# Kernel tuning notes

Hardware: AMD Instinct MI355X
Metric: run time of the kernel (lower is better)

## Reference

```python
import jax, jax.numpy as jnp
import numpy as np

FIRST_BIN = 0.0
LAST_BIN = 1.0
NBINS = 32
ER = 1.0
RATIO = 2.5066  # ~sqrt(2*pi), constant from the original module
SIGMA = (LAST_BIN - FIRST_BIN) / NBINS


def setup_inputs() -> dict:
    key = jax.random.key(0)
    x = jax.random.uniform(key, (8, 8, 256, 256), dtype=jnp.float32)
    bin_centers = jnp.linspace(FIRST_BIN, LAST_BIN, NBINS, dtype=jnp.float32)
    return {"x": x, "bin_centers": bin_centers}


def reference(x, bin_centers):
    # x: [B, C, H, W]; bin_centers: [nbins]
    B, C, H, W = x.shape
    nbins = bin_centers.shape[0]
    xc = jnp.clip(x, bin_centers[0], bin_centers[-1])
    # Gaussian soft binning: [B, C, H, W, nbins]
    diff = xc[..., None] - bin_centers
    w = (ER / RATIO) * jnp.exp(-(diff * diff) / (2.0 * SIGMA * SIGMA))
    # per-channel permute + concat == transpose then merge (C, nbins) -> C*nbins
    w = jnp.transpose(w, (0, 1, 4, 2, 3)).reshape(B, C * nbins, H, W)
    # pooling='sum' over dims [2,3] with keepdims
    return jnp.sum(w, axis=(2, 3), keepdims=True)
```

## Files before the change

### kernel.cpp

```cpp
#include <hip/hip_runtime.h>


#define NBINS        32
#define CHUNKS_PER_IMG 32
#define PX           2048

__device__ __forceinline__ float fast_exp2(float x) { return __builtin_amdgcn_exp2f(x); }

__global__ __launch_bounds__(256) void hist_partial(const float* __restrict__ x,
                                                    float* __restrict__ partial)
{
    __shared__ float2 sta[PX];
    __shared__ float  red[NBINS * 8];

    const int tid = threadIdx.x;
    const int bid = blockIdx.x;
    const int img   = bid >> 5;
    const int chunk = bid & (CHUNKS_PER_IMG - 1);
    const float* __restrict__ xp = x + (size_t)img * 65536 + (size_t)chunk * PX;

    const float C2L = -0.76863882f;

    #pragma unroll
    for (int k = 0; k < PX / 256; ++k) {
        int p = tid + 256 * k;
        float xv = xp[p];
        float xc = fminf(fmaxf(xv, 0.0f), 1.0f);
        float t  = xc * 31.0f;
        sta[p] = make_float2(t, C2L * t * t);
    }
    __syncthreads();

    const int j = tid & 31;
    const int g = tid >> 5;
    const float jf = (float)j;
    const float bj = 1.53727764f * jf;
    const float cj = C2L * jf * jf;

    const float4* __restrict__ sp = (const float4*)&sta[g * (PX >> 3)];
    float acc0 = 0.0f, acc1 = 0.0f;
    #pragma unroll 4
    for (int m = 0; m < (PX >> 4); ++m) {
        float4 v = sp[m];
        float a0 = fmaf(bj, v.x, v.y) + cj;
        float a1 = fmaf(bj, v.z, v.w) + cj;
        acc0 += fast_exp2(a0);
        acc1 += fast_exp2(a1);
    }

    red[j * 8 + g] = acc0 + acc1;
    __syncthreads();
    if (tid < NBINS) {
        float s = 0.0f;
        #pragma unroll
        for (int r = 0; r < 8; ++r) s += red[tid * 8 + r];
        partial[bid * NBINS + tid] = 0.39894678f * s;
    }
}

__global__ __launch_bounds__(256) void hist_reduce(const float* __restrict__ partial,
                                                   float* __restrict__ out)
{
    int o = blockIdx.x * 256 + threadIdx.x;
    int img = o >> 5;
    int bin = o & 31;
    float s = 0.0f;
    #pragma unroll
    for (int k = 0; k < CHUNKS_PER_IMG; ++k)
        s += partial[(img * CHUNKS_PER_IMG + k) * NBINS + bin];
    out[o] = s;
}

extern "C" void kernel_launch(void* const* d_in, const int* in_sizes, int n_in,
                              void* d_out, int out_size, void* d_ws, size_t ws_size,
                              hipStream_t stream)
{
    (void)in_sizes; (void)n_in; (void)out_size; (void)ws_size;
    const float* x = (const float*)d_in[0];
    float* out     = (float*)d_out;
    float* partial = (float*)d_ws;

    hist_partial<<<64 * CHUNKS_PER_IMG, 256, 0, stream>>>(x, partial);
    hist_reduce<<<8, 256, 0, stream>>>(partial, out);
}
```

Before: 79.19 us.

## Replace per-pixel Gaussian evaluation with fine sub-bin histogram and Taylor-corrected convolution

New measurement: 71.31 us. -10.0%, faster.

```diff
diff --git a/kernel.cpp b/kernel.cpp
--- a/kernel.cpp
+++ b/kernel.cpp
@@ -1,60 +1,75 @@
 #include <hip/hip_runtime.h>
 
 
-#define NBINS        32
-#define CHUNKS_PER_IMG 32
-#define PX           2048
+#define NBINS 32
+#define NBLK  512
+#define PXB   8192
+#define NSUB  2049
 
 __device__ __forceinline__ float fast_exp2(float x) { return __builtin_amdgcn_exp2f(x); }
 
 __global__ __launch_bounds__(256) void hist_partial(const float* __restrict__ x,
                                                     float* __restrict__ partial)
 {
-    __shared__ float2 sta[PX];
-    __shared__ float  red[NBINS * 8];
+    __shared__ unsigned long long hist[NSUB];
+    __shared__ float red[NBINS * 8];
 
     const int tid = threadIdx.x;
     const int bid = blockIdx.x;
-    const int img   = bid >> 5;
-    const int chunk = bid & (CHUNKS_PER_IMG - 1);
-    const float* __restrict__ xp = x + (size_t)img * 65536 + (size_t)chunk * PX;
 
-    const float C2L = -0.76863882f;
+    for (int i = tid; i < NSUB; i += 256) hist[i] = 0ull;
+    __syncthreads();
 
+    const float4* __restrict__ xv = (const float4*)(x + (size_t)bid * PXB);
     #pragma unroll
-    for (int k = 0; k < PX / 256; ++k) {
-        int p = tid + 256 * k;
-        float xv = xp[p];
-        float xc = fminf(fmaxf(xv, 0.0f), 1.0f);
-        float t  = xc * 31.0f;
-        sta[p] = make_float2(t, C2L * t * t);
+    for (int k = 0; k < PXB / 1024; ++k) {
+        float4 v = xv[tid + 256 * k];
+        #pragma unroll
+        for (int e = 0; e < 4; ++e) {
+            float xr = (e == 0) ? v.x : (e == 1) ? v.y : (e == 2) ? v.z : v.w;
+            float xc = fminf(fmaxf(xr, 0.0f), 1.0f);
+            float gf = xc * 2048.0f;
+            float sf = rintf(gf);
+            int   s  = (int)sf;
+            int   qi = (int)rintf((gf - sf) * 65536.0f) + 32768;
+            atomicAdd(&hist[s], ((unsigned long long)1 << 32) | (unsigned)qi);
+        }
     }
     __syncthreads();
 
     const int j = tid & 31;
     const int g = tid >> 5;
     const float jf = (float)j;
-    const float bj = 1.53727764f * jf;
-    const float cj = C2L * jf * jf;
 
-    const float4* __restrict__ sp = (const float4*)&sta[g * (PX >> 3)];
-    float acc0 = 0.0f, acc1 = 0.0f;
-    #pragma unroll 4
-    for (int m = 0; m < (PX >> 4); ++m) {
-        float4 v = sp[m];
-        float a0 = fmaf(bj, v.x, v.y) + cj;
-        float a1 = fmaf(bj, v.z, v.w) + cj;
-        acc0 += fast_exp2(a0);
-        acc1 += fast_exp2(a1);
+    const float DT  = 0.015136719f;
+    const float C2L = -0.7686388f;
+    const float M2C = -1.0655567f;
+    const float QS  = 2.3096800e-7f;
+    const float R0  = 0.39894678f;
+
+    int s_lo = (int)ceilf((jf - 4.5f) * 66.064516f);
+    int s_hi = (int)floorf((jf + 4.5f) * 66.064516f);
+    if (s_lo < 0) s_lo = 0;
+    if (s_hi > NSUB - 1) s_hi = NSUB - 1;
+
+    float acc = 0.0f;
+    for (int s = s_lo + g; s <= s_hi; s += 8) {
+        unsigned long long h = hist[s];
+        unsigned n  = (unsigned)(h >> 32);
+        int      sq = (int)((unsigned)h - (n << 15));
+        float nf  = (float)n;
+        float dqt = (float)sq * QS;
+        float u   = fmaf((float)s, DT, -jf);
+        float w   = fast_exp2(C2L * u * u);
+        acc += w * fmaf(M2C * u, dqt, nf);
     }
-
-    red[j * 8 + g] = acc0 + acc1;
+    red[j * 8 + g] = acc;
     __syncthreads();
     if (tid < NBINS) {
-        float s = 0.0f;
+        float ssum = 0.0f;
         #pragma unroll
-        for (int r = 0; r < 8; ++r) s += red[tid * 8 + r];
-        partial[bid * NBINS + tid] = 0.39894678f * s;
+        for (int r = 0; r < 8; ++r) ssum += red[tid * 8 + r];
+        partial[bid * NBINS + tid] = R0 * ssum;
     }
 }
 
@@ -66,8 +81,8 @@
     int bin = o & 31;
     float s = 0.0f;
     #pragma unroll
-    for (int k = 0; k < CHUNKS_PER_IMG; ++k)
-        s += partial[(img * CHUNKS_PER_IMG + k) * NBINS + bin];
+    for (int k = 0; k < NBLK / 64; ++k)
+        s += partial[(img * (NBLK / 64) + k) * NBINS + bin];
     out[o] = s;
 }
 
@@ -80,6 +95,6 @@
     float* out     = (float*)d_out;
     float* partial = (float*)d_ws;
 
-    hist_partial<<<64 * CHUNKS_PER_IMG, 256, 0, stream>>>(x, partial);
+    hist_partial<<<NBLK, 256, 0, stream>>>(x, partial);
     hist_reduce<<<8, 256, 0, stream>>>(partial, out);
 }
```
